# Kernel tuning notes

Measured on AMD Instinct MI355X. Metric: run time of the kernel, lower is better.

The kernel has to match this reference:

```python
import jax, jax.numpy as jnp
import numpy as np

K = 1024      # num_embeddings
D = 256       # embedding_dim
BETA = 0.25
DECAY = 0.99
EPS = 1e-05


def setup_inputs() -> dict:
    key = jax.random.key(0)
    k1, k2 = jax.random.split(key)
    z_e = jax.random.normal(k1, (32, D, 32, 32), dtype=jnp.float32)
    embedding = jax.random.normal(k2, (K, D), dtype=jnp.float32)
    ema_cluster_size = jnp.zeros((K,), dtype=jnp.float32)
    ema_w = embedding  # buffer initialized as a clone of the codebook
    return {"z_e": z_e, "embedding": embedding,
            "ema_cluster_size": ema_cluster_size, "ema_w": ema_w}


def reference(z_e, embedding, ema_cluster_size, ema_w):
    B, Dd, H, W = z_e.shape
    # (B, D, H, W) -> (N, D)
    flat_z = jnp.transpose(z_e, (0, 2, 3, 1)).reshape(-1, Dd)

    # L2 distance argmin (||z||^2 + ||e||^2 - 2 z.e)
    dist = (jnp.sum(flat_z * flat_z, axis=1, keepdims=True)
            + jnp.sum(embedding * embedding, axis=1)
            - 2.0 * flat_z @ embedding.T)
    indices = jnp.argmin(dist, axis=1)  # (N,)

    # EMA update (operates on detached values; buffers updated in-place in torch)
    flat_z_sg = jax.lax.stop_gradient(flat_z)
    cluster_size = jax.ops.segment_sum(
        jnp.ones_like(indices, dtype=z_e.dtype), indices, num_segments=K)
    new_ema_cluster_size = DECAY * ema_cluster_size + (1.0 - DECAY) * cluster_size
    dw = jax.ops.segment_sum(flat_z_sg, indices, num_segments=K)  # one_hot.T @ flat_z
    new_ema_w = DECAY * ema_w + (1.0 - DECAY) * dw
    new_embedding = new_ema_w / (new_ema_cluster_size + EPS)[:, None]

    # Gather uses the *updated* codebook (torch copies into the buffer first)
    z_q_flat = new_embedding[indices]                      # (N, D)
    z_q = jnp.transpose(z_q_flat.reshape(B, H, W, Dd), (0, 3, 1, 2))

    # Straight-through estimator + commitment loss
    z_q_st = z_e + jax.lax.stop_gradient(z_q - z_e)
    vq_loss = BETA * jnp.mean((z_e - jax.lax.stop_gradient(z_q)) ** 2)

    return (z_q_st, vq_loss, indices.reshape(B, H, W),
            new_embedding, new_ema_cluster_size, new_ema_w)
```

## Files before the change

### kernel.cpp

```cpp
#include <hip/hip_runtime.h>
#include <stdint.h>

#define N_ROWS 32768
#define K_CODES 1024
#define D_DIM 256
#define NELEM 8388608

#define WS_COUNTS 0
#define WS_LOSS 1030
#define WS_ENORM 263168
#define WS_ROWBEST_BYTES 1056768

#define O_ZQ 0
#define O_LOSS 8388608
#define O_IDX 8388609
#define O_EMB 8421377
#define O_CS 8683521
#define O_EMAW 8684545

#define EP_BYTE_OFF 33685520

typedef _Float16 half8 __attribute__((ext_vector_type(8)));
typedef float f32x16 __attribute__((ext_vector_type(16)));

__device__ __forceinline__ unsigned int fenc(float f) {
    unsigned int u = __float_as_uint(f);
    return (u & 0x80000000u) ? ~u : (u | 0x80000000u);
}
__device__ __forceinline__ unsigned long long umin64(unsigned long long a, unsigned long long b) {
    return a < b ? a : b;
}
__device__ __forceinline__ void gll16(const void* g, void* l) {
    __builtin_amdgcn_global_load_lds((const __attribute__((address_space(1))) void*)g,
                                     (__attribute__((address_space(3))) void*)l, 16, 0, 0);
}

__global__ __launch_bounds__(256) void k_conv_e(const float* __restrict__ emb,
                                                _Float16* __restrict__ Ep,
                                                float* __restrict__ enorm,
                                                float* __restrict__ ws) {
    int k = blockIdx.x, d = threadIdx.x;
    int gid = k * 256 + d;
    if (gid < 2048) ws[gid] = 0.0f;
    unsigned long long* rb = (unsigned long long*)((char*)ws + WS_ROWBEST_BYTES);
    if (gid < N_ROWS) rb[gid] = 0xFFFFFFFFFFFFFFFFull;

    float v = emb[k * 256 + d];
    _Float16 h = (_Float16)v;
    _Float16 l = (_Float16)(v - (float)h);
    int s = d >> 3, sub = d & 7;
    Ep[((size_t)s * 1024 + k) * 8 + sub] = h;
    Ep[((size_t)(32 + s) * 1024 + k) * 8 + sub] = l;
    float sq = v * v;
    #pragma unroll
    for (int off = 32; off >= 1; off >>= 1) sq += __shfl_down(sq, off, 64);
    __shared__ float red[4];
    if ((d & 63) == 0) red[d >> 6] = sq;
    __syncthreads();
    if (d == 0) enorm[k] = (red[0] + red[1]) + (red[2] + red[3]);
}

__global__ __launch_bounds__(256) void k_conv_z(const float* __restrict__ z_e,
                                                _Float16* __restrict__ Zp,
                                                float* __restrict__ lossacc) {
    __shared__ float lt[64 * 68];
    __shared__ float red[4];
    int t = threadIdx.x;
    int hw0 = blockIdx.x * 64, d0 = blockIdx.y * 64, b = blockIdx.z;
    const float* src = z_e + (size_t)b * 262144 + (size_t)d0 * 1024 + hw0;
    int dl = t >> 4, hl = (t & 15) * 4;
    float sq = 0.0f;
    #pragma unroll
    for (int i = 0; i < 4; i++) {
        int d = dl + i * 16;
        float4 v = *(const float4*)(src + (size_t)d * 1024 + hl);
        sq += v.x * v.x + v.y * v.y + v.z * v.z + v.w * v.w;
        lt[(hl + 0) * 68 + d] = v.x;
        lt[(hl + 1) * 68 + d] = v.y;
        lt[(hl + 2) * 68 + d] = v.z;
        lt[(hl + 3) * 68 + d] = v.w;
    }
    __syncthreads();
    int hr = t >> 2, seg = t & 3;
    int n = b * 1024 + hw0 + hr;
    int sg0 = (d0 >> 3) + seg * 2;
    half8 hi[2], lo[2];
    #pragma unroll
    for (int p = 0; p < 2; p++) {
        #pragma unroll
        for (int j = 0; j < 8; j++) {
            float v = lt[hr * 68 + seg * 16 + p * 8 + j];
            _Float16 h = (_Float16)v;
            hi[p][j] = h;
            lo[p][j] = (_Float16)(v - (float)h);
        }
    }
    *(half8*)(Zp + ((size_t)(sg0 + 0) * 32768 + n) * 8) = hi[0];
    *(half8*)(Zp + ((size_t)(sg0 + 1) * 32768 + n) * 8) = hi[1];
    *(half8*)(Zp + ((size_t)(32 + sg0) * 32768 + n) * 8) = lo[0];
    *(half8*)(Zp + ((size_t)(33 + sg0) * 32768 + n) * 8) = lo[1];
    #pragma unroll
    for (int off = 32; off >= 1; off >>= 1) sq += __shfl_down(sq, off, 64);
    if ((t & 63) == 0) red[t >> 6] = sq;
    __syncthreads();
    if (t == 0) atomicAdd(lossacc, (red[0] + red[1]) + (red[2] + red[3]));
}

__global__ __launch_bounds__(512) void k_mm(const _Float16* __restrict__ Zp,
                                            const _Float16* __restrict__ Ep,
                                            const float* __restrict__ enorm,
                                            unsigned long long* __restrict__ row_best) {
    __shared__ __align__(16) char smem[65536];

    int t = threadIdx.x;
    int lane = t & 63, wv = t >> 6;
    int b = blockIdx.x;
    int wgid = (b & 7) * 64 + (b >> 3);
    int rt = wgid >> 2;
    int ct = wgid & 3;
    int row0 = rt * 256, code0 = ct * 256;

    int wr = wv >> 2, wc = wv & 3;
    int m31 = lane & 31, ko = lane >> 5;

    f32x16 acc[4][2];
    #pragma unroll
    for (int m = 0; m < 4; m++)
        #pragma unroll
        for (int n = 0; n < 2; n++)
            #pragma unroll
            for (int r = 0; r < 16; r++) acc[m][n][r] = 0.0f;

    int sseg_st = wv >> 1;
    int rowbase = (wv & 1) * 128;
    const char* zgw = (const char*)Zp + ((size_t)row0 + rowbase + lane) * 16;
    const char* egw = (const char*)Ep + ((size_t)code0 + rowbase + lane) * 16;

    auto zsb = [](int tt) { return (tt < 16 ? tt : tt - 16) * 4; };
    auto esb = [](int tt) { return tt < 8 ? tt * 4 : (tt < 16 ? (tt - 8) * 4 : 32 + (tt - 16) * 4); };

    auto STAGE = [&](int c, int buf) {
        int zs = zsb(c) + sseg_st, es = esb(c) + sseg_st;
        const char* zg = zgw + (size_t)zs * 32768 * 16;
        const char* eg = egw + (size_t)es * 1024 * 16;
        char* zl = smem + buf * 32768 + sseg_st * 4096 + rowbase * 16;
        char* el = smem + buf * 32768 + 16384 + sseg_st * 4096 + rowbase * 16;
        gll16(zg, zl);
        gll16(zg + 64 * 16, zl + 64 * 16);
        gll16(eg, el);
        gll16(eg + 64 * 16, el + 64 * 16);
    };

    STAGE(0, 0);
    STAGE(1, 1);
    asm volatile("s_waitcnt vmcnt(4)" ::: "memory");
    __builtin_amdgcn_s_barrier();
    asm volatile("" ::: "memory");

    for (int c = 0; c < 24; c++) {
        const _Float16* Za = (const _Float16*)(smem + (c & 1) * 32768);
        const _Float16* Ea = (const _Float16*)(smem + (c & 1) * 32768 + 16384);
        __builtin_amdgcn_s_setprio(1);
        #pragma unroll
        for (int ks = 0; ks < 2; ks++) {
            int sseg = 2 * ks + ko;
            half8 a0 = *(const half8*)(Za + (sseg * 256 + wr * 128 +  0 + m31) * 8);
            half8 a1 = *(const half8*)(Za + (sseg * 256 + wr * 128 + 32 + m31) * 8);
            half8 a2 = *(const half8*)(Za + (sseg * 256 + wr * 128 + 64 + m31) * 8);
            half8 a3 = *(const half8*)(Za + (sseg * 256 + wr * 128 + 96 + m31) * 8);
            half8 b0 = *(const half8*)(Ea + (sseg * 256 + wc * 64 +  0 + m31) * 8);
            half8 b1 = *(const half8*)(Ea + (sseg * 256 + wc * 64 + 32 + m31) * 8);
            acc[0][0] = __builtin_amdgcn_mfma_f32_32x32x16_f16(a0, b0, acc[0][0], 0, 0, 0);
            acc[0][1] = __builtin_amdgcn_mfma_f32_32x32x16_f16(a0, b1, acc[0][1], 0, 0, 0);
            acc[1][0] = __builtin_amdgcn_mfma_f32_32x32x16_f16(a1, b0, acc[1][0], 0, 0, 0);
            acc[1][1] = __builtin_amdgcn_mfma_f32_32x32x16_f16(a1, b1, acc[1][1], 0, 0, 0);
            acc[2][0] = __builtin_amdgcn_mfma_f32_32x32x16_f16(a2, b0, acc[2][0], 0, 0, 0);
            acc[2][1] = __builtin_amdgcn_mfma_f32_32x32x16_f16(a2, b1, acc[2][1], 0, 0, 0);
            acc[3][0] = __builtin_amdgcn_mfma_f32_32x32x16_f16(a3, b0, acc[3][0], 0, 0, 0);
            acc[3][1] = __builtin_amdgcn_mfma_f32_32x32x16_f16(a3, b1, acc[3][1], 0, 0, 0);
        }
        __builtin_amdgcn_s_setprio(0);
        asm volatile("s_waitcnt lgkmcnt(0)" ::: "memory");
        __builtin_amdgcn_s_barrier();
        if (c < 22) STAGE(c + 2, c & 1);
        if (c < 23) {
            if (c < 22) asm volatile("s_waitcnt vmcnt(4)" ::: "memory");
            else        asm volatile("s_waitcnt vmcnt(0)" ::: "memory");
            __builtin_amdgcn_s_barrier();
            asm volatile("" ::: "memory");
        }
    }

    unsigned long long* slot = (unsigned long long*)smem;
    float en0 = enorm[code0 + wc * 64 + m31];
    float en1 = enorm[code0 + wc * 64 + 32 + m31];
    unsigned int col0 = code0 + wc * 64 + m31;
    unsigned int col1 = col0 + 32;

    if (wc == 0) {
        #pragma unroll
        for (int m = 0; m < 4; m++)
            #pragma unroll
            for (int j = 0; j < 16; j++) {
                int row = wr * 128 + m * 32 + 4 * ko + (j & 3) + 8 * (j >> 2);
                unsigned long long p0 = ((unsigned long long)fenc(en0 - 2.0f * acc[m][0][j]) << 32) | col0;
                unsigned long long p1 = ((unsigned long long)fenc(en1 - 2.0f * acc[m][1][j]) << 32) | col1;
                slot[row * 32 + ((m31 + row) & 31)] = umin64(p0, p1);
            }
    }
    __syncthreads();
    if (wc != 0) {
        #pragma unroll
        for (int m = 0; m < 4; m++)
            #pragma unroll
            for (int j = 0; j < 16; j++) {
                int row = wr * 128 + m * 32 + 4 * ko + (j & 3) + 8 * (j >> 2);
                unsigned long long p0 = ((unsigned long long)fenc(en0 - 2.0f * acc[m][0][j]) << 32) | col0;
                unsigned long long p1 = ((unsigned long long)fenc(en1 - 2.0f * acc[m][1][j]) << 32) | col1;
                atomicMin(&slot[row * 32 + ((m31 + row) & 31)], umin64(p0, p1));
            }
    }
    __syncthreads();
    if (t < 256) {
        unsigned long long mm = slot[t * 32 + (t & 31)];
        #pragma unroll
        for (int i = 1; i < 32; i++) mm = umin64(mm, slot[t * 32 + ((i + t) & 31)]);
        atomicMin(&row_best[row0 + t], mm);
    }
}

__global__ __launch_bounds__(512) void k_dw(const float* __restrict__ z_e,
                                            const unsigned long long* __restrict__ rb,
                                            float* __restrict__ counts,
                                            float* __restrict__ dw,
                                            float* __restrict__ out) {
    __shared__ float acc[K_CODES];
    int t = threadIdx.x;
    int d = blockIdx.x;
    #pragma unroll
    for (int j = 0; j < 2; j++) acc[j * 512 + t] = 0.0f;
    __syncthreads();
    for (int b = 0; b < 32; b++) {
        ulonglong2 rr = *(const ulonglong2*)(rb + (size_t)b * 1024 + t * 2);
        float2 v = *(const float2*)(z_e + (size_t)b * 262144 + (size_t)d * 1024 + t * 2);
        atomicAdd(&acc[(int)(rr.x & 0xFFFFFFFFull)], v.x);
        atomicAdd(&acc[(int)(rr.y & 0xFFFFFFFFull)], v.y);
    }
    __syncthreads();
    float* pr = dw + (size_t)d * 1024;
    #pragma unroll
    for (int j = 0; j < 2; j++) pr[j * 512 + t] = acc[j * 512 + t];
    __syncthreads();
    #pragma unroll
    for (int j = 0; j < 2; j++) acc[j * 512 + t] = 0.0f;
    __syncthreads();
    if (t < 128) {
        int i = d * 128 + t;
        int id = (int)(rb[i] & 0xFFFFFFFFull);
        out[O_IDX + i] = (float)id;
        atomicAdd(&acc[id], 1.0f);
    }
    __syncthreads();
    #pragma unroll
    for (int j = 0; j < 2; j++) {
        float h = acc[j * 512 + t];
        if (h != 0.0f) atomicAdd(&counts[j * 512 + t], h);
    }
}

__global__ __launch_bounds__(256) void k_red(const float* __restrict__ dw,
                                             const float* __restrict__ ema_cs,
                                             const float* __restrict__ ema_w,
                                             const float* __restrict__ counts,
                                             float* __restrict__ lossacc,
                                             float* __restrict__ out) {
    __shared__ float tile[64 * 69];
    __shared__ float csl[64];
    __shared__ float craw[64];
    __shared__ float red[4];
    int t = threadIdx.x;
    int k0 = blockIdx.x * 64, d0 = blockIdx.y * 64;
    int dr = t >> 4, kc = t & 15;
    if (t < 64) {
        float c = counts[k0 + t];
        craw[t] = c;
        csl[t] = 0.99f * ema_cs[k0 + t] + 0.01f * c;
    }
    #pragma unroll
    for (int q = 0; q < 4; q++) {
        float4 v = *(const float4*)(dw + (size_t)(d0 + dr + 16 * q) * 1024 + k0 + kc * 4);
        float* p = tile + (dr + 16 * q) * 69 + kc * 4;
        p[0] = v.x; p[1] = v.y; p[2] = v.z; p[3] = v.w;
    }
    __syncthreads();
    int kk = t >> 2, dq = t & 3;
    int k = k0 + kk;
    float inv = 1.0f / (csl[kk] + 1e-5f);
    float cr = craw[kk];
    float lterm = 0.0f;
    #pragma unroll
    for (int j4 = 0; j4 < 4; j4++) {
        int dd = dq * 16 + j4 * 4;
        size_t kd = (size_t)k * 256 + d0 + dd;
        float4 w = *(const float4*)(ema_w + kd);
        float s0 = tile[(dd + 0) * 69 + kk];
        float s1 = tile[(dd + 1) * 69 + kk];
        float s2 = tile[(dd + 2) * 69 + kk];
        float s3 = tile[(dd + 3) * 69 + kk];
        float4 nw;
        nw.x = 0.99f * w.x + 0.01f * s0;
        nw.y = 0.99f * w.y + 0.01f * s1;
        nw.z = 0.99f * w.z + 0.01f * s2;
        nw.w = 0.99f * w.w + 0.01f * s3;
        *(float4*)(out + O_EMAW + kd) = nw;
        float4 ne = {nw.x * inv, nw.y * inv, nw.z * inv, nw.w * inv};
        *(float4*)(out + O_EMB + kd) = ne;
        lterm += ne.x * (cr * ne.x - 2.0f * s0);
        lterm += ne.y * (cr * ne.y - 2.0f * s1);
        lterm += ne.z * (cr * ne.z - 2.0f * s2);
        lterm += ne.w * (cr * ne.w - 2.0f * s3);
    }
    if (blockIdx.y == 0 && t < 64) out[O_CS + k0 + t] = csl[t];
    #pragma unroll
    for (int off = 32; off >= 1; off >>= 1) lterm += __shfl_down(lterm, off, 64);
    if ((t & 63) == 0) red[t >> 6] = lterm;
    __syncthreads();
    if (t == 0) atomicAdd(lossacc, (red[0] + red[1]) + (red[2] + red[3]));
}

__global__ __launch_bounds__(256) void k_bcast(const unsigned long long* __restrict__ rb,
                                               const float* __restrict__ lossacc,
                                               float* __restrict__ out) {
    __shared__ float lt[64 * 68];
    __shared__ int sid[64];
    int t = threadIdx.x;
    int hw0 = blockIdx.x * 64, d0 = blockIdx.y * 64, b = blockIdx.z;
    if (t < 64) sid[t] = (int)(rb[b * 1024 + hw0 + t] & 0xFFFFFFFFull);
    __syncthreads();
    int r = t >> 2, c = t & 3;
    const float* nrow = out + O_EMB + (size_t)sid[r] * 256 + d0;
    #pragma unroll
    for (int it = 0; it < 4; it++) {
        int dd = it * 16 + c * 4;
        float4 q = *(const float4*)(nrow + dd);
        float* p = lt + r * 68 + dd;
        p[0] = q.x; p[1] = q.y; p[2] = q.z; p[3] = q.w;
    }
    __syncthreads();
    int dl = t >> 4, hl = (t & 15) * 4;
    float* dst = out + O_ZQ + (size_t)b * 262144 + (size_t)d0 * 1024 + hw0;
    #pragma unroll
    for (int i = 0; i < 4; i++) {
        int d = dl + i * 16;
        float4 w;
        w.x = lt[(hl + 0) * 68 + d];
        w.y = lt[(hl + 1) * 68 + d];
        w.z = lt[(hl + 2) * 68 + d];
        w.w = lt[(hl + 3) * 68 + d];
        *(float4*)(dst + (size_t)d * 1024 + hl) = w;
    }
    if (blockIdx.x == 0 && blockIdx.y == 0 && blockIdx.z == 0 && t == 0)
        out[O_LOSS] = lossacc[0] * 2.9802322387695312e-08f;
}

extern "C" void kernel_launch(void* const* d_in, const int* in_sizes, int n_in,
                              void* d_out, int out_size, void* d_ws, size_t ws_size,
                              hipStream_t stream) {
    const float* z_e = (const float*)d_in[0];
    const float* emb = (const float*)d_in[1];
    const float* ema_cs = (const float*)d_in[2];
    const float* ema_w = (const float*)d_in[3];
    float* out = (float*)d_out;
    float* ws = (float*)d_ws;

    float* counts = ws + WS_COUNTS;
    float* lossacc = ws + WS_LOSS;
    float* enorm = ws + WS_ENORM;
    unsigned long long* row_best = (unsigned long long*)((char*)d_ws + WS_ROWBEST_BYTES);

    _Float16* Zp = (_Float16*)d_out;
    _Float16* Ep = (_Float16*)((char*)d_out + EP_BYTE_OFF);
    float* dw = (float*)d_out;

    k_conv_e<<<1024, 256, 0, stream>>>(emb, Ep, enorm, ws);
    k_conv_z<<<dim3(16, 4, 32), 256, 0, stream>>>(z_e, Zp, lossacc);
    k_mm<<<512, 512, 0, stream>>>(Zp, Ep, enorm, row_best);
    k_dw<<<256, 512, 0, stream>>>(z_e, row_best, counts, dw, out);
    k_red<<<dim3(16, 4), 256, 0, stream>>>(dw, ema_cs, ema_w, counts, lossacc, out);
    k_bcast<<<dim3(16, 4, 32), 256, 0, stream>>>(row_best, lossacc, out);
}
```

Baseline: 240.9 us.

## Software-pipeline LDS fragment reads in GEMM and precompute int32 indices

The GEMM main loop now double-buffers its register fragments. The second k-slice is read from LDS while the first slice's MFMAs run, and the next chunk's first slice is prefetched after the barrier, with sched_barrier placed to preserve that ordering. A new small kernel extracts int32 indices and the cluster histogram from the packed 64-bit row_best. k_dw and k_bcast then read 4-byte indices instead of 8-byte words. This adds one extra launch and higher register pressure in exchange for hiding LDS latency and reducing index traffic.

```diff
diff --git a/kernel.cpp b/kernel.cpp
--- a/kernel.cpp
+++ b/kernel.cpp
@@ -10,6 +10,7 @@
 #define WS_LOSS 1030
 #define WS_ENORM 263168
 #define WS_ROWBEST_BYTES 1056768
+#define WS_IDX_BYTES 1318912
 
 #define O_ZQ 0
 #define O_LOSS 8388608
@@ -105,6 +106,27 @@
     __syncthreads();
     if (t == 0) atomicAdd(lossacc, (red[0] + red[1]) + (red[2] + red[3]));
 }
+
+#define READ_FRAGS(AF, BF, ZA, EA, KS) do {                                   \
+    const int _ss = 2 * (KS) + ko;                                            \
+    AF[0] = *(const half8*)((ZA) + (_ss * 256 + wr * 128 +  0 + m31) * 8);    \
+    AF[1] = *(const half8*)((ZA) + (_ss * 256 + wr * 128 + 32 + m31) * 8);    \
+    AF[2] = *(const half8*)((ZA) + (_ss * 256 + wr * 128 + 64 + m31) * 8);    \
+    AF[3] = *(const half8*)((ZA) + (_ss * 256 + wr * 128 + 96 + m31) * 8);    \
+    BF[0] = *(const half8*)((EA) + (_ss * 256 + wc * 64 +  0 + m31) * 8);     \
+    BF[1] = *(const half8*)((EA) + (_ss * 256 + wc * 64 + 32 + m31) * 8);     \
+} while (0)
+
+#define DO_MFMA(AF, BF) do {                                                  \
+    acc[0][0] = __builtin_amdgcn_mfma_f32_32x32x16_f16(AF[0], BF[0], acc[0][0], 0, 0, 0); \
+    acc[0][1] = __builtin_amdgcn_mfma_f32_32x32x16_f16(AF[0], BF[1], acc[0][1], 0, 0, 0); \
+    acc[1][0] = __builtin_amdgcn_mfma_f32_32x32x16_f16(AF[1], BF[0], acc[1][0], 0, 0, 0); \
+    acc[1][1] = __builtin_amdgcn_mfma_f32_32x32x16_f16(AF[1], BF[1], acc[1][1], 0, 0, 0); \
+    acc[2][0] = __builtin_amdgcn_mfma_f32_32x32x16_f16(AF[2], BF[0], acc[2][0], 0, 0, 0); \
+    acc[2][1] = __builtin_amdgcn_mfma_f32_32x32x16_f16(AF[2], BF[1], acc[2][1], 0, 0, 0); \
+    acc[3][0] = __builtin_amdgcn_mfma_f32_32x32x16_f16(AF[3], BF[0], acc[3][0], 0, 0, 0); \
+    acc[3][1] = __builtin_amdgcn_mfma_f32_32x32x16_f16(AF[3], BF[1], acc[3][1], 0, 0, 0); \
+} while (0)
 
 __global__ __launch_bounds__(512) void k_mm(const _Float16* __restrict__ Zp,
                                             const _Float16* __restrict__ Ep,
@@ -151,36 +173,26 @@
         gll16(eg + 64 * 16, el + 64 * 16);
     };
 
+    half8 af0[4], bf0[2], af1[4], bf1[2];
+
     STAGE(0, 0);
     STAGE(1, 1);
     asm volatile("s_waitcnt vmcnt(4)" ::: "memory");
     __builtin_amdgcn_s_barrier();
     asm volatile("" ::: "memory");
+    READ_FRAGS(af0, bf0, (const _Float16*)smem, (const _Float16*)(smem + 16384), 0);
 
     for (int c = 0; c < 24; c++) {
         const _Float16* Za = (const _Float16*)(smem + (c & 1) * 32768);
         const _Float16* Ea = (const _Float16*)(smem + (c & 1) * 32768 + 16384);
+        READ_FRAGS(af1, bf1, Za, Ea, 1);
+        asm volatile("s_waitcnt lgkmcnt(6)" ::: "memory");
+        __builtin_amdgcn_sched_barrier(0);
         __builtin_amdgcn_s_setprio(1);
-        #pragma unroll
-        for (int ks = 0; ks < 2; ks++) {
-            int sseg = 2 * ks + ko;
-            half8 a0 = *(const half8*)(Za + (sseg * 256 + wr * 128 +  0 + m31) * 8);
-            half8 a1 = *(const half8*)(Za + (sseg * 256 + wr * 128 + 32 + m31) * 8);
-            half8 a2 = *(const half8*)(Za + (sseg * 256 + wr * 128 + 64 + m31) * 8);
-            half8 a3 = *(const half8*)(Za + (sseg * 256 + wr * 128 + 96 + m31) * 8);
-            half8 b0 = *(const half8*)(Ea + (sseg * 256 + wc * 64 +  0 + m31) * 8);
-            half8 b1 = *(const half8*)(Ea + (sseg * 256 + wc * 64 + 32 + m31) * 8);
-            acc[0][0] = __builtin_amdgcn_mfma_f32_32x32x16_f16(a0, b0, acc[0][0], 0, 0, 0);
-            acc[0][1] = __builtin_amdgcn_mfma_f32_32x32x16_f16(a0, b1, acc[0][1], 0, 0, 0);
-            acc[1][0] = __builtin_amdgcn_mfma_f32_32x32x16_f16(a1, b0, acc[1][0], 0, 0, 0);
-            acc[1][1] = __builtin_amdgcn_mfma_f32_32x32x16_f16(a1, b1, acc[1][1], 0, 0, 0);
-            acc[2][0] = __builtin_amdgcn_mfma_f32_32x32x16_f16(a2, b0, acc[2][0], 0, 0, 0);
-            acc[2][1] = __builtin_amdgcn_mfma_f32_32x32x16_f16(a2, b1, acc[2][1], 0, 0, 0);
-            acc[3][0] = __builtin_amdgcn_mfma_f32_32x32x16_f16(a3, b0, acc[3][0], 0, 0, 0);
-            acc[3][1] = __builtin_amdgcn_mfma_f32_32x32x16_f16(a3, b1, acc[3][1], 0, 0, 0);
-        }
+        DO_MFMA(af0, bf0);
         __builtin_amdgcn_s_setprio(0);
         asm volatile("s_waitcnt lgkmcnt(0)" ::: "memory");
+        __builtin_amdgcn_sched_barrier(0);
         __builtin_amdgcn_s_barrier();
         if (c < 22) STAGE(c + 2, c & 1);
         if (c < 23) {
@@ -188,7 +200,14 @@
             else        asm volatile("s_waitcnt vmcnt(0)" ::: "memory");
             __builtin_amdgcn_s_barrier();
             asm volatile("" ::: "memory");
+            const _Float16* Zn = (const _Float16*)(smem + ((c + 1) & 1) * 32768);
+            const _Float16* En = (const _Float16*)(smem + ((c + 1) & 1) * 32768 + 16384);
+            READ_FRAGS(af0, bf0, Zn, En, 0);
         }
+        __builtin_amdgcn_sched_barrier(0);
+        __builtin_amdgcn_s_setprio(1);
+        DO_MFMA(af1, bf1);
+        __builtin_amdgcn_s_setprio(0);
     }
 
     unsigned long long* slot = (unsigned long long*)smem;
@@ -229,11 +248,31 @@
     }
 }
 
+__global__ __launch_bounds__(256) void k_fin_idx(const unsigned long long* __restrict__ rb,
+                                                 int* __restrict__ idxs,
+                                                 float* __restrict__ counts,
+                                                 float* __restrict__ out) {
+    __shared__ float hist[K_CODES];
+    int t = threadIdx.x;
+    #pragma unroll
+    for (int j = 0; j < 4; j++) hist[j * 256 + t] = 0.0f;
+    __syncthreads();
+    int i = blockIdx.x * 256 + t;
+    int id = (int)(rb[i] & 0xFFFFFFFFull);
+    idxs[i] = id;
+    out[O_IDX + i] = (float)id;
+    atomicAdd(&hist[id], 1.0f);
+    __syncthreads();
+    #pragma unroll
+    for (int j = 0; j < 4; j++) {
+        float h = hist[j * 256 + t];
+        if (h != 0.0f) atomicAdd(&counts[j * 256 + t], h);
+    }
+}
+
 __global__ __launch_bounds__(512) void k_dw(const float* __restrict__ z_e,
-                                            const unsigned long long* __restrict__ rb,
-                                            float* __restrict__ counts,
-                                            float* __restrict__ dw,
-                                            float* __restrict__ out) {
+                                            const int* __restrict__ idxs,
+                                            float* __restrict__ dw) {
     __shared__ float acc[K_CODES];
     int t = threadIdx.x;
     int d = blockIdx.x;
@@ -241,31 +280,15 @@
     for (int j = 0; j < 2; j++) acc[j * 512 + t] = 0.0f;
     __syncthreads();
     for (int b = 0; b < 32; b++) {
-        ulonglong2 rr = *(const ulonglong2*)(rb + (size_t)b * 1024 + t * 2);
+        int2 id2 = *(const int2*)(idxs + b * 1024 + t * 2);
         float2 v = *(const float2*)(z_e + (size_t)b * 262144 + (size_t)d * 1024 + t * 2);
-        atomicAdd(&acc[(int)(rr.x & 0xFFFFFFFFull)], v.x);
-        atomicAdd(&acc[(int)(rr.y & 0xFFFFFFFFull)], v.y);
+        atomicAdd(&acc[id2.x], v.x);
+        atomicAdd(&acc[id2.y], v.y);
     }
     __syncthreads();
     float* pr = dw + (size_t)d * 1024;
     #pragma unroll
     for (int j = 0; j < 2; j++) pr[j * 512 + t] = acc[j * 512 + t];
-    __syncthreads();
-    #pragma unroll
-    for (int j = 0; j < 2; j++) acc[j * 512 + t] = 0.0f;
-    __syncthreads();
-    if (t < 128) {
-        int i = d * 128 + t;
-        int id = (int)(rb[i] & 0xFFFFFFFFull);
-        out[O_IDX + i] = (float)id;
-        atomicAdd(&acc[id], 1.0f);
-    }
-    __syncthreads();
-    #pragma unroll
-    for (int j = 0; j < 2; j++) {
-        float h = acc[j * 512 + t];
-        if (h != 0.0f) atomicAdd(&counts[j * 512 + t], h);
-    }
 }
 
 __global__ __launch_bounds__(256) void k_red(const float* __restrict__ dw,
@@ -328,14 +351,14 @@
     if (t == 0) atomicAdd(lossacc, (red[0] + red[1]) + (red[2] + red[3]));
 }
 
-__global__ __launch_bounds__(256) void k_bcast(const unsigned long long* __restrict__ rb,
+__global__ __launch_bounds__(256) void k_bcast(const int* __restrict__ idxs,
                                                const float* __restrict__ lossacc,
                                                float* __restrict__ out) {
     __shared__ float lt[64 * 68];
     __shared__ int sid[64];
     int t = threadIdx.x;
     int hw0 = blockIdx.x * 64, d0 = blockIdx.y * 64, b = blockIdx.z;
-    if (t < 64) sid[t] = (int)(rb[b * 1024 + hw0 + t] & 0xFFFFFFFFull);
+    if (t < 64) sid[t] = idxs[b * 1024 + hw0 + t];
     __syncthreads();
     int r = t >> 2, c = t & 3;
     const float* nrow = out + O_EMB + (size_t)sid[r] * 256 + d0;
@@ -377,6 +400,7 @@
     float* lossacc = ws + WS_LOSS;
     float* enorm = ws + WS_ENORM;
     unsigned long long* row_best = (unsigned long long*)((char*)d_ws + WS_ROWBEST_BYTES);
+    int* idxs = (int*)((char*)d_ws + WS_IDX_BYTES);
 
     _Float16* Zp = (_Float16*)d_out;
     _Float16* Ep = (_Float16*)((char*)d_out + EP_BYTE_OFF);
@@ -385,7 +409,8 @@
     k_conv_e<<<1024, 256, 0, stream>>>(emb, Ep, enorm, ws);
     k_conv_z<<<dim3(16, 4, 32), 256, 0, stream>>>(z_e, Zp, lossacc);
     k_mm<<<512, 512, 0, stream>>>(Zp, Ep, enorm, row_best);
-    k_dw<<<256, 512, 0, stream>>>(z_e, row_best, counts, dw, out);
+    k_fin_idx<<<128, 256, 0, stream>>>(row_best, idxs, counts, out);
+    k_dw<<<256, 512, 0, stream>>>(z_e, idxs, dw);
     k_red<<<dim3(16, 4), 256, 0, stream>>>(dw, ema_cs, ema_w, counts, lossacc, out);
-    k_bcast<<<dim3(16, 4, 32), 256, 0, stream>>>(row_best, lossacc, out);
-}
+    k_bcast<<<dim3(16, 4, 32), 256, 0, stream>>>(idxs, lossacc, out);
+}
```

Result: no change. 239.9 us (-0.4%).
